# Optimization experiments

Measured on AMD Instinct MI355X. Metric: run time of the kernel, lower is better.

Reference implementation:

```python
import jax, jax.numpy as jnp
import numpy as np

B, C, N, DI, DC = 64, 32, 1152, 8, 16
ROUTINGS = 3


def squash(x, axis=-1):
    sq = jnp.sum(x * x, axis=axis, keepdims=True)
    scale = sq / (1.0 + sq) / jnp.sqrt(sq + 1e-07)
    return scale * x


def setup_inputs() -> dict:
    key = jax.random.key(0)
    k1, k2 = jax.random.split(key)
    inputs = jax.random.normal(k1, (B, N, DI), dtype=jnp.float32)
    # Xavier-uniform init for W[n_caps, n_in, d_cap, d_in]; fan computed over last two dims
    limit = float(np.sqrt(6.0 / (DC + DI)))
    W = jax.random.uniform(k2, (C, N, DC, DI), dtype=jnp.float32, minval=-limit, maxval=limit)
    return {"inputs": inputs, "W": W}


def reference(inputs, W):
    # inputs_hat[b,c,n,i] = sum_j W[c,n,i,j] * inputs[b,n,j]
    inputs_hat = jnp.einsum('cnij,bnj->bcni', W, inputs)  # [B,C,N,DC]
    b = jnp.zeros((B, C, N), dtype=inputs_hat.dtype)
    outputs = None
    for i in range(ROUTINGS):
        c = jax.nn.softmax(b, axis=1)                      # over output capsules
        s = jnp.einsum('bcn,bcni->bci', c, inputs_hat)     # weighted sum over input caps
        outputs = squash(s)                                # [B,C,DC]
        if i < ROUTINGS - 1:
            agreement = jnp.einsum('bci,bcni->bcn', outputs, inputs_hat)
            b = b + agreement
    return outputs
```

## Files before the change

### kernel.cpp

```cpp
#include <hip/hip_runtime.h>
#include <hip/hip_bf16.h>
#include <hip/hip_fp16.h>

#define B_  64
#define C_  32
#define N_  1152
#define DI_ 8
#define DC_ 16
#define STH 512

#define HCH 2
#define HSLOT 192
#define NOCT 24

#define FCH 3
#define FSLOT 128

static __device__ __forceinline__ unsigned pkh(float a, float b) {
    __half2 t = __float22half2_rn(make_float2(a, b));
    return *reinterpret_cast<unsigned*>(&t);
}
static __device__ __forceinline__ float2 uph(unsigned u) {
    __half2 h; *reinterpret_cast<unsigned*>(&h) = u;
    return __half22float2(h);
}

__global__ __launch_bounds__(STH, 4) void caps_hat(
    const float* __restrict__ X, const float* __restrict__ W,
    uint4* __restrict__ hatg, float* __restrict__ p1)
{
    __shared__ float wlds[HCH * 64 * 64];

    const int xcd  = blockIdx.x & 7;
    const int k    = blockIdx.x >> 3;
    const int bg   = k & 3;
    const int slot = 24 * xcd + (k >> 2);

    const int tid  = threadIdx.x;
    const int lane = tid & 63;
    const int c    = lane & 31;
    const int h    = lane >> 5;
    const int le   = 2 * c + h;
    const int sw   = c & 7;
    const int wu   = __builtin_amdgcn_readfirstlane(tid) >> 6;
    const int bl0  = wu * 2;

    float acc[2][8];
#pragma unroll
    for (int bq = 0; bq < 2; bq++)
#pragma unroll
        for (int r = 0; r < 8; r++) acc[bq][r] = 0.f;

    for (int cc = 0; cc < 3; cc++) {
        if (cc) __syncthreads();
        const int n0 = (slot + cc * HSLOT) * HCH;

#pragma unroll
        for (int G = tid; G < HCH * 1024; G += STH) {
            const int nl = G >> 10, f = (G >> 4) & 63, q = G & 15;
            const int wc = f >> 1, wh = f & 1;
            const float4 v = *(const float4*)(W + (size_t)(wc * N_ + n0 + nl) * 128 + wh * 64 + q * 4);
            *(float4*)(wlds + (nl * 64 + f) * 64 + (q ^ (wc & 7)) * 4) = v;
        }
        __syncthreads();

#pragma unroll
        for (int nl = 0; nl < HCH; nl++) {
            float4 xa[2], xb[2];
#pragma unroll
            for (int bq = 0; bq < 2; bq++) {
                const float* xp = X + ((size_t)(bg * 16 + bl0 + bq) * N_ + n0 + nl) * DI_;
                xa[bq] = *(const float4*)xp;
                xb[bq] = *(const float4*)(xp + 4);
            }
            uint4 hq[2];
            const float* frag = wlds + (nl * 64 + le) * 64;
#pragma unroll
            for (int rp = 0; rp < 4; rp++) {
                const int r0 = 2 * rp, r1 = r0 + 1;
                const int pa0 = ((2 * r0) ^ sw) * 4;
                const int pb0 = pa0 ^ 4;
                const int pa1 = ((2 * r1) ^ sw) * 4;
                const int pb1 = pa1 ^ 4;
                const float4 wa0 = *(const float4*)(frag + pa0);
                const float4 wb0 = *(const float4*)(frag + pb0);
                const float4 wa1 = *(const float4*)(frag + pa1);
                const float4 wb1 = *(const float4*)(frag + pb1);
#pragma unroll
                for (int bq = 0; bq < 2; bq++) {
                    const float hv0 = wa0.x*xa[bq].x + wa0.y*xa[bq].y + wa0.z*xa[bq].z + wa0.w*xa[bq].w
                                    + wb0.x*xb[bq].x + wb0.y*xb[bq].y + wb0.z*xb[bq].z + wb0.w*xb[bq].w;
                    const float hv1 = wa1.x*xa[bq].x + wa1.y*xa[bq].y + wa1.z*xa[bq].z + wa1.w*xa[bq].w
                                    + wb1.x*xb[bq].x + wb1.y*xb[bq].y + wb1.z*xb[bq].z + wb1.w*xb[bq].w;
                    acc[bq][r0] += hv0;
                    acc[bq][r1] += hv1;
                    (&hq[bq].x)[rp] = pkh(hv0, hv1);
                }
            }
#pragma unroll
            for (int bq = 0; bq < 2; bq++) {
                const int b = bg * 16 + bl0 + bq;
                hatg[(size_t)(b * N_ + n0 + nl) * 64 + le] = hq[bq];
            }
        }
    }

    float* pout = p1 + (size_t)(bg * HSLOT + slot) * (16 * 512);
#pragma unroll
    for (int bq = 0; bq < 2; bq++) {
        float* pb = pout + (bl0 + bq) * 512 + le * 8;
        *(float4*)pb       = make_float4(acc[bq][0]*0.03125f, acc[bq][1]*0.03125f,
                                         acc[bq][2]*0.03125f, acc[bq][3]*0.03125f);
        *(float4*)(pb + 4) = make_float4(acc[bq][4]*0.03125f, acc[bq][5]*0.03125f,
                                         acc[bq][6]*0.03125f, acc[bq][7]*0.03125f);
    }
}

__global__ __launch_bounds__(STH, 4) void caps_route(
    const uint4* __restrict__ hatg, const float* __restrict__ accb,
    float* __restrict__ p2)
{
    __shared__ float red[8 * 512];
    const int xcd  = blockIdx.x & 7;
    const int rest = blockIdx.x >> 3;
    const int ug   = rest % 3;
    const int b    = rest / 3;
    const int u    = 8 * ug + xcd;
    const int tid  = threadIdx.x;
    const int w    = tid >> 6;
    const int lane = tid & 63;
    const int c    = lane & 31;
    const int h    = lane >> 5;
    const int le   = 2 * c + h;

    const float* ap = accb + (size_t)b * 512 + le * 8;
    const float4 a0 = *(const float4*)ap;
    const float4 a1 = *(const float4*)(ap + 4);

    const uint4* hb = hatg + (size_t)(b * N_ + u * 48) * 64 + le;

    uint4 v[6];
#pragma unroll
    for (int m = 0; m < 6; m++)
        v[m] = hb[(size_t)(w + 8 * m) * 64];

    float lg[6], sm[6];
#pragma unroll
    for (int m = 0; m < 6; m++) {
        const float2 f0 = uph(v[m].x);
        const float2 f1 = uph(v[m].y);
        const float2 f2 = uph(v[m].z);
        const float2 f3 = uph(v[m].w);
        lg[m] = f0.x*a0.x + f0.y*a0.y + f1.x*a0.z + f1.y*a0.w
              + f2.x*a1.x + f2.y*a1.y + f3.x*a1.z + f3.y*a1.w;
    }
#pragma unroll
    for (int m = 0; m < 6; m++) lg[m] += __shfl_xor(lg[m], 32, 64);
#pragma unroll
    for (int m = 0; m < 6; m++) { lg[m] = __expf(lg[m]); sm[m] = lg[m]; }
#pragma unroll
    for (int d = 16; d >= 1; d >>= 1)
#pragma unroll
        for (int m = 0; m < 6; m++) sm[m] += __shfl_xor(sm[m], d, 64);

    float acc[8] = {0.f,0.f,0.f,0.f,0.f,0.f,0.f,0.f};
#pragma unroll
    for (int m = 0; m < 6; m++) {
        const float sc = lg[m] * __builtin_amdgcn_rcpf(sm[m]);
        const float2 f0 = uph(v[m].x);
        const float2 f1 = uph(v[m].y);
        const float2 f2 = uph(v[m].z);
        const float2 f3 = uph(v[m].w);
        acc[0] += sc * f0.x; acc[1] += sc * f0.y;
        acc[2] += sc * f1.x; acc[3] += sc * f1.y;
        acc[4] += sc * f2.x; acc[5] += sc * f2.y;
        acc[6] += sc * f3.x; acc[7] += sc * f3.y;
    }
    *(float4*)(red + w * 512 + le * 8)     = make_float4(acc[0], acc[1], acc[2], acc[3]);
    *(float4*)(red + w * 512 + le * 8 + 4) = make_float4(acc[4], acc[5], acc[6], acc[7]);
    __syncthreads();
    float vs = 0.f;
#pragma unroll
    for (int s = 0; s < 8; s++) vs += red[s * 512 + tid];
    p2[(size_t)(b * NOCT + u) * 512 + tid] = vs;
}

__global__ __launch_bounds__(512) void caps_r1(
    const float* __restrict__ p1, float* __restrict__ accb,
    float* __restrict__ out, int t)
{
    const int b   = blockIdx.x >> 2;
    const int q   = blockIdx.x & 3;
    const int tid = threadIdx.x;
    const int e   = q * 128 + (tid >> 2);
    const int p   = tid & 3;
    const int bg  = b >> 4, bl = b & 15;
    const float* base = p1 + (size_t)bg * HSLOT * 8192 + (size_t)bl * 512 + e;
    float v = 0.f;
#pragma unroll 8
    for (int ch = p; ch < HSLOT; ch += 4)
        v += base[(size_t)ch * 8192];
    v += __shfl_xor(v, 1, 64);
    v += __shfl_xor(v, 2, 64);
    float sq = v * v;
#pragma unroll
    for (int m = 4; m <= 32; m <<= 1) sq += __shfl_xor(sq, m, 64);
    const float scale = sq / (1.f + sq) * rsqrtf(sq + 1e-7f);
    const float ov = v * scale;
    if (p == 0) {
        const int oidx = b * 512 + e;
        if (t == 2) out[oidx] = ov;
        else        accb[oidx] = (t == 0) ? ov : (accb[oidx] + ov);
    }
}

__global__ __launch_bounds__(512) void caps_r2(
    const float* __restrict__ p2, float* __restrict__ accb,
    float* __restrict__ out, int t)
{
    const int b = blockIdx.x;
    const int e = threadIdx.x;
    const float* base = p2 + (size_t)b * (NOCT * 512) + e;
    float v = 0.f;
#pragma unroll
    for (int s = 0; s < NOCT; s++) v += base[s * 512];
    float sq = v * v;
#pragma unroll
    for (int m = 1; m <= 8; m <<= 1) sq += __shfl_xor(sq, m, 64);
    const float scale = sq / (1.f + sq) * rsqrtf(sq + 1e-7f);
    const float ov = v * scale;
    const int oidx = b * 512 + e;
    if (t == 2) out[oidx] = ov;
    else        accb[oidx] += ov;
}

__global__ __launch_bounds__(STH, 2) void caps_s_fb(
    const float* __restrict__ X, const float* __restrict__ W,
    const float* __restrict__ aout, float* __restrict__ partials, int t)
{
    __shared__ float wlds[FCH * 64 * 64];
    __shared__ float xlds[FCH * 16 * 8];
    const int bg = blockIdx.x & 3, slot = blockIdx.x >> 2;
    const int tid = threadIdx.x, w = tid >> 6, lane = tid & 63;
    const int c = lane & 31, h = lane >> 5, bl0 = w * 2, sw = c & 7;
    float areg[2][8] = {};
    if (t > 0) {
#pragma unroll
        for (int bq = 0; bq < 2; bq++) {
            const float* ap = aout + (size_t)(bg * 16 + bl0 + bq) * 512 + c * 16 + h * 8;
            const float4 a0 = *(const float4*)ap; const float4 a1 = *(const float4*)(ap + 4);
            areg[bq][0]=a0.x; areg[bq][1]=a0.y; areg[bq][2]=a0.z; areg[bq][3]=a0.w;
            areg[bq][4]=a1.x; areg[bq][5]=a1.y; areg[bq][6]=a1.z; areg[bq][7]=a1.w;
        }
    }
    float acc[2][8];
#pragma unroll
    for (int bq = 0; bq < 2; bq++)
#pragma unroll
        for (int r = 0; r < 8; r++) acc[bq][r] = 0.f;
    for (int cc = 0; cc < 3; cc++) {
        if (cc) __syncthreads();
        const int n0 = (slot + cc * FSLOT) * FCH;
        for (int G = tid; G < FCH * 1024; G += STH) {
            const int nl = G >> 10, f = (G >> 4) & 63, q = G & 15;
            const int wc = f >> 1, wh = f & 1;
            const float4 v = *(const float4*)(W + (size_t)(wc * N_ + n0 + nl) * 128 + wh * 64 + q * 4);
            *(float4*)(wlds + (nl * 64 + f) * 64 + (q ^ (wc & 7)) * 4) = v;
        }
        if (tid < FCH * 32) {
            const int nl = tid >> 5, bl = (tid >> 1) & 15, qx = tid & 1;
            const float4 v = *(const float4*)(X + (size_t)((bg * 16 + bl) * N_ + n0 + nl) * DI_ + qx * 4);
            *(float4*)(xlds + (nl * 16 + bl) * 8 + qx * 4) = v;
        }
        __syncthreads();
#pragma unroll
        for (int nl = 0; nl < FCH; nl++) {
            float4 xa[2], xb[2];
#pragma unroll
            for (int bq = 0; bq < 2; bq++) {
                const float* xp = xlds + (nl * 16 + bl0 + bq) * 8;
                xa[bq] = *(const float4*)xp; xb[bq] = *(const float4*)(xp + 4);
            }
            float hat[2][8];
            const float* frag = wlds + (nl * 64 + 2 * c + h) * 64;
#pragma unroll
            for (int r = 0; r < 8; r++) {
                const int pa = ((2 * r) ^ sw) * 4; const int pb = pa ^ 4;
                const float4 wa = *(const float4*)(frag + pa);
                const float4 wb = *(const float4*)(frag + pb);
#pragma unroll
                for (int bq = 0; bq < 2; bq++)
                    hat[bq][r] = wa.x*xa[bq].x + wa.y*xa[bq].y + wa.z*xa[bq].z + wa.w*xa[bq].w
                               + wb.x*xb[bq].x + wb.y*xb[bq].y + wb.z*xb[bq].z + wb.w*xb[bq].w;
            }
#pragma unroll
            for (int bq = 0; bq < 2; bq++) {
                float softc;
                if (t > 0) {
                    float lg = hat[bq][0]*areg[bq][0] + hat[bq][1]*areg[bq][1]
                             + hat[bq][2]*areg[bq][2] + hat[bq][3]*areg[bq][3]
                             + hat[bq][4]*areg[bq][4] + hat[bq][5]*areg[bq][5]
                             + hat[bq][6]*areg[bq][6] + hat[bq][7]*areg[bq][7];
                    lg += __shfl_xor(lg, 32, 64);
                    const float e = __expf(lg);
                    float s = e;
#pragma unroll
                    for (int m = 16; m >= 1; m >>= 1) s += __shfl_xor(s, m, 64);
                    softc = e / s;
                } else softc = 1.0f / 32.0f;
#pragma unroll
                for (int r = 0; r < 8; r++) acc[bq][r] += softc * hat[bq][r];
            }
        }
    }
    float* pout = partials + (size_t)(bg * FSLOT + slot) * (16 * 512);
#pragma unroll
    for (int bq = 0; bq < 2; bq++) {
        float* pb = pout + (bl0 + bq) * 512 + c * 16 + h * 8;
        *(float4*)pb       = make_float4(acc[bq][0], acc[bq][1], acc[bq][2], acc[bq][3]);
        *(float4*)(pb + 4) = make_float4(acc[bq][4], acc[bq][5], acc[bq][6], acc[bq][7]);
    }
}

__global__ __launch_bounds__(256) void caps_r1_fb(
    const float* __restrict__ partials, float* __restrict__ accb,
    float* __restrict__ out, int t)
{
    const int b   = blockIdx.x >> 2;
    const int q   = blockIdx.x & 3;
    const int tid = threadIdx.x;
    const int e   = q * 128 + (tid >> 1);
    const int p   = tid & 1;
    const int bg  = b >> 4, bl = b & 15;
    const float* base = partials + (size_t)bg * FSLOT * 8192 + (size_t)bl * 512 + e;
    float v = 0.f;
#pragma unroll 8
    for (int ch = p; ch < FSLOT; ch += 2)
        v += base[(size_t)ch * 8192];
    v += __shfl_xor(v, 1, 64);
    float sq = v * v;
#pragma unroll
    for (int m = 2; m <= 16; m <<= 1) sq += __shfl_xor(sq, m, 64);
    const float scale = sq / (1.f + sq) * rsqrtf(sq + 1e-7f);
    const float ov = v * scale;
    if (p == 0) {
        const int oidx = b * 512 + e;
        if (t == 2) out[oidx] = ov;
        else        accb[oidx] = (t == 0) ? ov : (accb[oidx] + ov);
    }
}

extern "C" void kernel_launch(void* const* d_in, const int* in_sizes, int n_in,
                              void* d_out, int out_size, void* d_ws, size_t ws_size,
                              hipStream_t stream) {
    const float* X = (const float*)d_in[0];
    const float* W = (const float*)d_in[1];
    float* out = (float*)d_out;

    const size_t hat_b = (size_t)B_ * N_ * 512 * 2;
    const size_t p1_b  = (size_t)4 * HSLOT * 8192 * 4;
    const size_t p2_b  = (size_t)B_ * NOCT * 512 * 4;
    const size_t acc_b = (size_t)B_ * 512 * 4;

    if (ws_size >= hat_b + p1_b + p2_b + acc_b) {
        char* ws = (char*)d_ws;
        uint4* hatg = (uint4*)ws;
        float* p1   = (float*)(ws + hat_b);
        float* p2   = (float*)(ws + hat_b + p1_b);
        float* accb = (float*)(ws + hat_b + p1_b + p2_b);
        caps_hat  <<<768, STH, 0, stream>>>(X, W, hatg, p1);
        caps_r1   <<<256, 512, 0, stream>>>(p1, accb, out, 0);
        caps_route<<<B_ * NOCT, STH, 0, stream>>>(hatg, accb, p2);
        caps_r2   <<<64, 512, 0, stream>>>(p2, accb, out, 1);
        caps_route<<<B_ * NOCT, STH, 0, stream>>>(hatg, accb, p2);
        caps_r2   <<<64, 512, 0, stream>>>(p2, accb, out, 2);
    } else {
        float* partials = (float*)d_ws;
        float* accb = partials + (size_t)512 * 8192;
        for (int t = 0; t < 3; t++) {
            caps_s_fb<<<512, STH, 0, stream>>>(X, W, accb, partials, t);
            caps_r1_fb<<<256, 256, 0, stream>>>(partials, accb, out, t);
        }
    }
}
```

Measured before the change: 128.9 us.

## Recompute prediction vectors each routing pass instead of storing fp16 hat tensor

Drops the materialized fp16 inputs_hat buffer and the separate route/reduce kernels. Each of the three routing iterations now reruns a fused kernel that recomputes hat from W and X, applies the softmax-weighted accumulation in registers, and writes partials for the existing r1 reduction. This trades the large hat write and two hat reads for re-reading W (about 4.7 MB) and redoing the matvec in every pass. It also removes the fp16 rounding of hat.

```diff
diff --git a/kernel.cpp b/kernel.cpp
--- a/kernel.cpp
+++ b/kernel.cpp
@@ -11,23 +11,13 @@
 
 #define HCH 2
 #define HSLOT 192
-#define NOCT 24
 
 #define FCH 3
 #define FSLOT 128
 
-static __device__ __forceinline__ unsigned pkh(float a, float b) {
-    __half2 t = __float22half2_rn(make_float2(a, b));
-    return *reinterpret_cast<unsigned*>(&t);
-}
-static __device__ __forceinline__ float2 uph(unsigned u) {
-    __half2 h; *reinterpret_cast<unsigned*>(&h) = u;
-    return __half22float2(h);
-}
-
-__global__ __launch_bounds__(STH, 4) void caps_hat(
+__global__ __launch_bounds__(STH, 4) void caps_pass(
     const float* __restrict__ X, const float* __restrict__ W,
-    uint4* __restrict__ hatg, float* __restrict__ p1)
+    const float* __restrict__ accb, float* __restrict__ p1, int t)
 {
     __shared__ float wlds[HCH * 64 * 64];
 
@@ -45,6 +35,18 @@
     const int wu   = __builtin_amdgcn_readfirstlane(tid) >> 6;
     const int bl0  = wu * 2;
 
+    float areg[2][8];
+    if (t > 0) {
+#pragma unroll
+        for (int bq = 0; bq < 2; bq++) {
+            const float* ap = accb + (size_t)(bg * 16 + bl0 + bq) * 512 + le * 8;
+            const float4 a0 = *(const float4*)ap;
+            const float4 a1 = *(const float4*)(ap + 4);
+            areg[bq][0]=a0.x; areg[bq][1]=a0.y; areg[bq][2]=a0.z; areg[bq][3]=a0.w;
+            areg[bq][4]=a1.x; areg[bq][5]=a1.y; areg[bq][6]=a1.z; areg[bq][7]=a1.w;
+        }
+    }
+
     float acc[2][8];
 #pragma unroll
     for (int bq = 0; bq < 2; bq++)
@@ -73,7 +75,7 @@
                 xa[bq] = *(const float4*)xp;
                 xb[bq] = *(const float4*)(xp + 4);
             }
-            uint4 hq[2];
+            float hat[2][8];
             const float* frag = wlds + (nl * 64 + le) * 64;
 #pragma unroll
             for (int rp = 0; rp < 4; rp++) {
@@ -88,19 +90,43 @@
                 const float4 wb1 = *(const float4*)(frag + pb1);
 #pragma unroll
                 for (int bq = 0; bq < 2; bq++) {
-                    const float hv0 = wa0.x*xa[bq].x + wa0.y*xa[bq].y + wa0.z*xa[bq].z + wa0.w*xa[bq].w
-                                    + wb0.x*xb[bq].x + wb0.y*xb[bq].y + wb0.z*xb[bq].z + wb0.w*xb[bq].w;
-                    const float hv1 = wa1.x*xa[bq].x + wa1.y*xa[bq].y + wa1.z*xa[bq].z + wa1.w*xa[bq].w
-                                    + wb1.x*xb[bq].x + wb1.y*xb[bq].y + wb1.z*xb[bq].z + wb1.w*xb[bq].w;
-                    acc[bq][r0] += hv0;
-                    acc[bq][r1] += hv1;
-                    (&hq[bq].x)[rp] = pkh(hv0, hv1);
+                    hat[bq][r0] = wa0.x*xa[bq].x + wa0.y*xa[bq].y + wa0.z*xa[bq].z + wa0.w*xa[bq].w
+                                + wb0.x*xb[bq].x + wb0.y*xb[bq].y + wb0.z*xb[bq].z + wb0.w*xb[bq].w;
+                    hat[bq][r1] = wa1.x*xa[bq].x + wa1.y*xa[bq].y + wa1.z*xa[bq].z + wa1.w*xa[bq].w
+                                + wb1.x*xb[bq].x + wb1.y*xb[bq].y + wb1.z*xb[bq].z + wb1.w*xb[bq].w;
                 }
             }
-#pragma unroll
-            for (int bq = 0; bq < 2; bq++) {
-                const int b = bg * 16 + bl0 + bq;
-                hatg[(size_t)(b * N_ + n0 + nl) * 64 + le] = hq[bq];
+            if (t == 0) {
+#pragma unroll
+                for (int bq = 0; bq < 2; bq++)
+#pragma unroll
+                    for (int r = 0; r < 8; r++) acc[bq][r] += 0.03125f * hat[bq][r];
+            } else {
+                float lg0 = hat[0][0]*areg[0][0] + hat[0][1]*areg[0][1]
+                          + hat[0][2]*areg[0][2] + hat[0][3]*areg[0][3]
+                          + hat[0][4]*areg[0][4] + hat[0][5]*areg[0][5]
+                          + hat[0][6]*areg[0][6] + hat[0][7]*areg[0][7];
+                float lg1 = hat[1][0]*areg[1][0] + hat[1][1]*areg[1][1]
+                          + hat[1][2]*areg[1][2] + hat[1][3]*areg[1][3]
+                          + hat[1][4]*areg[1][4] + hat[1][5]*areg[1][5]
+                          + hat[1][6]*areg[1][6] + hat[1][7]*areg[1][7];
+                lg0 += __shfl_xor(lg0, 32, 64);
+                lg1 += __shfl_xor(lg1, 32, 64);
+                const float e0 = __expf(lg0);
+                const float e1 = __expf(lg1);
+                float s0 = e0, s1 = e1;
+#pragma unroll
+                for (int m = 16; m >= 1; m >>= 1) {
+                    s0 += __shfl_xor(s0, m, 64);
+                    s1 += __shfl_xor(s1, m, 64);
+                }
+                const float sc0 = e0 * __builtin_amdgcn_rcpf(s0);
+                const float sc1 = e1 * __builtin_amdgcn_rcpf(s1);
+#pragma unroll
+                for (int r = 0; r < 8; r++) {
+                    acc[0][r] += sc0 * hat[0][r];
+                    acc[1][r] += sc1 * hat[1][r];
+                }
             }
         }
     }
@@ -109,80 +135,9 @@
 #pragma unroll
     for (int bq = 0; bq < 2; bq++) {
         float* pb = pout + (bl0 + bq) * 512 + le * 8;
-        *(float4*)pb       = make_float4(acc[bq][0]*0.03125f, acc[bq][1]*0.03125f,
-                                         acc[bq][2]*0.03125f, acc[bq][3]*0.03125f);
-        *(float4*)(pb + 4) = make_float4(acc[bq][4]*0.03125f, acc[bq][5]*0.03125f,
-                                         acc[bq][6]*0.03125f, acc[bq][7]*0.03125f);
-    }
-}
-
-__global__ __launch_bounds__(STH, 4) void caps_route(
-    const uint4* __restrict__ hatg, const float* __restrict__ accb,
-    float* __restrict__ p2)
-{
-    __shared__ float red[8 * 512];
-    const int xcd  = blockIdx.x & 7;
-    const int rest = blockIdx.x >> 3;
-    const int ug   = rest % 3;
-    const int b    = rest / 3;
-    const int u    = 8 * ug + xcd;
-    const int tid  = threadIdx.x;
-    const int w    = tid >> 6;
-    const int lane = tid & 63;
-    const int c    = lane & 31;
-    const int h    = lane >> 5;
-    const int le   = 2 * c + h;
-
-    const float* ap = accb + (size_t)b * 512 + le * 8;
-    const float4 a0 = *(const float4*)ap;
-    const float4 a1 = *(const float4*)(ap + 4);
-
-    const uint4* hb = hatg + (size_t)(b * N_ + u * 48) * 64 + le;
-
-    uint4 v[6];
-#pragma unroll
-    for (int m = 0; m < 6; m++)
-        v[m] = hb[(size_t)(w + 8 * m) * 64];
-
-    float lg[6], sm[6];
-#pragma unroll
-    for (int m = 0; m < 6; m++) {
-        const float2 f0 = uph(v[m].x);
-        const float2 f1 = uph(v[m].y);
-        const float2 f2 = uph(v[m].z);
-        const float2 f3 = uph(v[m].w);
-        lg[m] = f0.x*a0.x + f0.y*a0.y + f1.x*a0.z + f1.y*a0.w
-              + f2.x*a1.x + f2.y*a1.y + f3.x*a1.z + f3.y*a1.w;
-    }
-#pragma unroll
-    for (int m = 0; m < 6; m++) lg[m] += __shfl_xor(lg[m], 32, 64);
-#pragma unroll
-    for (int m = 0; m < 6; m++) { lg[m] = __expf(lg[m]); sm[m] = lg[m]; }
-#pragma unroll
-    for (int d = 16; d >= 1; d >>= 1)
-#pragma unroll
-        for (int m = 0; m < 6; m++) sm[m] += __shfl_xor(sm[m], d, 64);
-
-    float acc[8] = {0.f,0.f,0.f,0.f,0.f,0.f,0.f,0.f};
-#pragma unroll
-    for (int m = 0; m < 6; m++) {
-        const float sc = lg[m] * __builtin_amdgcn_rcpf(sm[m]);
-        const float2 f0 = uph(v[m].x);
-        const float2 f1 = uph(v[m].y);
-        const float2 f2 = uph(v[m].z);
-        const float2 f3 = uph(v[m].w);
-        acc[0] += sc * f0.x; acc[1] += sc * f0.y;
-        acc[2] += sc * f1.x; acc[3] += sc * f1.y;
-        acc[4] += sc * f2.x; acc[5] += sc * f2.y;
-        acc[6] += sc * f3.x; acc[7] += sc * f3.y;
-    }
-    *(float4*)(red + w * 512 + le * 8)     = make_float4(acc[0], acc[1], acc[2], acc[3]);
-    *(float4*)(red + w * 512 + le * 8 + 4) = make_float4(acc[4], acc[5], acc[6], acc[7]);
-    __syncthreads();
-    float vs = 0.f;
-#pragma unroll
-    for (int s = 0; s < 8; s++) vs += red[s * 512 + tid];
-    p2[(size_t)(b * NOCT + u) * 512 + tid] = vs;
+        *(float4*)pb       = make_float4(acc[bq][0], acc[bq][1], acc[bq][2], acc[bq][3]);
+        *(float4*)(pb + 4) = make_float4(acc[bq][4], acc[bq][5], acc[bq][6], acc[bq][7]);
+    }
 }
 
 __global__ __launch_bounds__(512) void caps_r1(
@@ -214,26 +169,6 @@
     }
 }
 
-__global__ __launch_bounds__(512) void caps_r2(
-    const float* __restrict__ p2, float* __restrict__ accb,
-    float* __restrict__ out, int t)
-{
-    const int b = blockIdx.x;
-    const int e = threadIdx.x;
-    const float* base = p2 + (size_t)b * (NOCT * 512) + e;
-    float v = 0.f;
-#pragma unroll
-    for (int s = 0; s < NOCT; s++) v += base[s * 512];
-    float sq = v * v;
-#pragma unroll
-    for (int m = 1; m <= 8; m <<= 1) sq += __shfl_xor(sq, m, 64);
-    const float scale = sq / (1.f + sq) * rsqrtf(sq + 1e-7f);
-    const float ov = v * scale;
-    const int oidx = b * 512 + e;
-    if (t == 2) out[oidx] = ov;
-    else        accb[oidx] += ov;
-}
-
 __global__ __launch_bounds__(STH, 2) void caps_s_fb(
     const float* __restrict__ X, const float* __restrict__ W,
     const float* __restrict__ aout, float* __restrict__ partials, int t)
@@ -357,23 +292,17 @@
     const float* W = (const float*)d_in[1];
     float* out = (float*)d_out;
 
-    const size_t hat_b = (size_t)B_ * N_ * 512 * 2;
     const size_t p1_b  = (size_t)4 * HSLOT * 8192 * 4;
-    const size_t p2_b  = (size_t)B_ * NOCT * 512 * 4;
     const size_t acc_b = (size_t)B_ * 512 * 4;
 
-    if (ws_size >= hat_b + p1_b + p2_b + acc_b) {
+    if (ws_size >= p1_b + acc_b) {
         char* ws = (char*)d_ws;
-        uint4* hatg = (uint4*)ws;
-        float* p1   = (float*)(ws + hat_b);
-        float* p2   = (float*)(ws + hat_b + p1_b);
-        float* accb = (float*)(ws + hat_b + p1_b + p2_b);
-        caps_hat  <<<768, STH, 0, stream>>>(X, W, hatg, p1);
-        caps_r1   <<<256, 512, 0, stream>>>(p1, accb, out, 0);
-        caps_route<<<B_ * NOCT, STH, 0, stream>>>(hatg, accb, p2);
-        caps_r2   <<<64, 512, 0, stream>>>(p2, accb, out, 1);
-        caps_route<<<B_ * NOCT, STH, 0, stream>>>(hatg, accb, p2);
-        caps_r2   <<<64, 512, 0, stream>>>(p2, accb, out, 2);
+        float* p1   = (float*)ws;
+        float* accb = (float*)(ws + p1_b);
+        for (int t = 0; t < 3; t++) {
+            caps_pass<<<768, STH, 0, stream>>>(X, W, accb, p1, t);
+            caps_r1  <<<256, 512, 0, stream>>>(p1, accb, out, t);
+        }
     } else {
         float* partials = (float*)d_ws;
         float* accb = partials + (size_t)512 * 8192;
```

New measurement: 209.8 us. +62.8%, slower.

## Prefetch next W chunk into registers, store iteration-1 partials as fp16

Applied to the files above, without the earlier changes.

caps_hat now loads the next W chunk into registers while it computes on the current chunk in LDS, then writes it to LDS after a barrier. The aim is to hide global-load latency behind the FMA work. The per-slot partial sums p1 are stored as packed half2 instead of float, and caps_r1 is reworked to read and reduce half2 pairs, which halves that traffic. Launch bounds drop from 4 to 2 waves-per-EU hint, giving more registers at some cost in occupancy, and fp16 partials lose precision.

```diff
diff --git a/kernel.cpp b/kernel.cpp
--- a/kernel.cpp
+++ b/kernel.cpp
@@ -25,9 +25,9 @@
     return __half22float2(h);
 }
 
-__global__ __launch_bounds__(STH, 4) void caps_hat(
+__global__ __launch_bounds__(STH, 2) void caps_hat(
     const float* __restrict__ X, const float* __restrict__ W,
-    uint4* __restrict__ hatg, float* __restrict__ p1)
+    uint4* __restrict__ hatg, __half2* __restrict__ p1)
 {
     __shared__ float wlds[HCH * 64 * 64];
 
@@ -45,24 +45,42 @@
     const int wu   = __builtin_amdgcn_readfirstlane(tid) >> 6;
     const int bl0  = wu * 2;
 
+    const int g_nl[4] = { (tid) >> 10, (tid + 512) >> 10, (tid + 1024) >> 10, (tid + 1536) >> 10 };
+    const int g_f [4] = { (tid >> 4) & 63, ((tid + 512) >> 4) & 63, ((tid + 1024) >> 4) & 63, ((tid + 1536) >> 4) & 63 };
+    const int g_q  = tid & 15;
+
     float acc[2][8];
 #pragma unroll
     for (int bq = 0; bq < 2; bq++)
 #pragma unroll
         for (int r = 0; r < 8; r++) acc[bq][r] = 0.f;
 
+    float4 wreg[4];
+    {
+        const int n0 = slot * HCH;
+#pragma unroll
+        for (int i = 0; i < 4; i++) {
+            const int wc = g_f[i] >> 1, wh = g_f[i] & 1;
+            wreg[i] = *(const float4*)(W + (size_t)(wc * N_ + n0 + g_nl[i]) * 128 + wh * 64 + g_q * 4);
+        }
+#pragma unroll
+        for (int i = 0; i < 4; i++) {
+            const int wc = g_f[i] >> 1;
+            *(float4*)(wlds + (g_nl[i] * 64 + g_f[i]) * 64 + (g_q ^ (wc & 7)) * 4) = wreg[i];
+        }
+    }
+    __syncthreads();
+
     for (int cc = 0; cc < 3; cc++) {
-        if (cc) __syncthreads();
+        if (cc < 2) {
+            const int n0 = (slot + (cc + 1) * HSLOT) * HCH;
+#pragma unroll
+            for (int i = 0; i < 4; i++) {
+                const int wc = g_f[i] >> 1, wh = g_f[i] & 1;
+                wreg[i] = *(const float4*)(W + (size_t)(wc * N_ + n0 + g_nl[i]) * 128 + wh * 64 + g_q * 4);
+            }
+        }
         const int n0 = (slot + cc * HSLOT) * HCH;
-
-#pragma unroll
-        for (int G = tid; G < HCH * 1024; G += STH) {
-            const int nl = G >> 10, f = (G >> 4) & 63, q = G & 15;
-            const int wc = f >> 1, wh = f & 1;
-            const float4 v = *(const float4*)(W + (size_t)(wc * N_ + n0 + nl) * 128 + wh * 64 + q * 4);
-            *(float4*)(wlds + (nl * 64 + f) * 64 + (q ^ (wc & 7)) * 4) = v;
-        }
-        __syncthreads();
 
 #pragma unroll
         for (int nl = 0; nl < HCH; nl++) {
@@ -103,20 +121,31 @@
                 hatg[(size_t)(b * N_ + n0 + nl) * 64 + le] = hq[bq];
             }
         }
-    }
-
-    float* pout = p1 + (size_t)(bg * HSLOT + slot) * (16 * 512);
+
+        __syncthreads();
+        if (cc < 2) {
+#pragma unroll
+            for (int i = 0; i < 4; i++) {
+                const int wc = g_f[i] >> 1;
+                *(float4*)(wlds + (g_nl[i] * 64 + g_f[i]) * 64 + (g_q ^ (wc & 7)) * 4) = wreg[i];
+            }
+            __syncthreads();
+        }
+    }
+
+    __half2* pout = p1 + (size_t)(bg * HSLOT + slot) * (16 * 256);
 #pragma unroll
     for (int bq = 0; bq < 2; bq++) {
-        float* pb = pout + (bl0 + bq) * 512 + le * 8;
-        *(float4*)pb       = make_float4(acc[bq][0]*0.03125f, acc[bq][1]*0.03125f,
-                                         acc[bq][2]*0.03125f, acc[bq][3]*0.03125f);
-        *(float4*)(pb + 4) = make_float4(acc[bq][4]*0.03125f, acc[bq][5]*0.03125f,
-                                         acc[bq][6]*0.03125f, acc[bq][7]*0.03125f);
-    }
-}
-
-__global__ __launch_bounds__(STH, 4) void caps_route(
+        uint4 st;
+        st.x = pkh(acc[bq][0]*0.03125f, acc[bq][1]*0.03125f);
+        st.y = pkh(acc[bq][2]*0.03125f, acc[bq][3]*0.03125f);
+        st.z = pkh(acc[bq][4]*0.03125f, acc[bq][5]*0.03125f);
+        st.w = pkh(acc[bq][6]*0.03125f, acc[bq][7]*0.03125f);
+        *(uint4*)(pout + (bl0 + bq) * 256 + le * 4) = st;
+    }
+}
+
+__global__ __launch_bounds__(STH, 2) void caps_route(
     const uint4* __restrict__ hatg, const float* __restrict__ accb,
     float* __restrict__ p2)
 {
@@ -186,31 +215,36 @@
 }
 
 __global__ __launch_bounds__(512) void caps_r1(
-    const float* __restrict__ p1, float* __restrict__ accb,
+    const __half2* __restrict__ p1, float* __restrict__ accb,
     float* __restrict__ out, int t)
 {
     const int b   = blockIdx.x >> 2;
     const int q   = blockIdx.x & 3;
     const int tid = threadIdx.x;
-    const int e   = q * 128 + (tid >> 2);
-    const int p   = tid & 3;
+    const int ep  = tid >> 3;
+    const int p   = tid & 7;
     const int bg  = b >> 4, bl = b & 15;
-    const float* base = p1 + (size_t)bg * HSLOT * 8192 + (size_t)bl * 512 + e;
-    float v = 0.f;
+    const __half2* base = p1 + (size_t)bg * HSLOT * 4096 + bl * 256 + (q * 64 + ep);
+    float vx = 0.f, vy = 0.f;
 #pragma unroll 8
-    for (int ch = p; ch < HSLOT; ch += 4)
-        v += base[(size_t)ch * 8192];
-    v += __shfl_xor(v, 1, 64);
-    v += __shfl_xor(v, 2, 64);
-    float sq = v * v;
-#pragma unroll
-    for (int m = 4; m <= 32; m <<= 1) sq += __shfl_xor(sq, m, 64);
+    for (int ch = p; ch < HSLOT; ch += 8) {
+        const float2 f = __half22float2(base[(size_t)ch * 4096]);
+        vx += f.x; vy += f.y;
+    }
+    vx += __shfl_xor(vx, 1, 64);  vy += __shfl_xor(vy, 1, 64);
+    vx += __shfl_xor(vx, 2, 64);  vy += __shfl_xor(vy, 2, 64);
+    vx += __shfl_xor(vx, 4, 64);  vy += __shfl_xor(vy, 4, 64);
+    float sq = vx * vx + vy * vy;
+    sq += __shfl_xor(sq, 8, 64);
+    sq += __shfl_xor(sq, 16, 64);
+    sq += __shfl_xor(sq, 32, 64);
     const float scale = sq / (1.f + sq) * rsqrtf(sq + 1e-7f);
-    const float ov = v * scale;
     if (p == 0) {
-        const int oidx = b * 512 + e;
-        if (t == 2) out[oidx] = ov;
-        else        accb[oidx] = (t == 0) ? ov : (accb[oidx] + ov);
+        const int oidx = b * 512 + q * 128 + ep * 2;
+        const float ox = vx * scale, oy = vy * scale;
+        if (t == 2) { out[oidx] = ox; out[oidx + 1] = oy; }
+        else if (t == 0) { accb[oidx] = ox; accb[oidx + 1] = oy; }
+        else { accb[oidx] += ox; accb[oidx + 1] += oy; }
     }
 }
 
@@ -358,16 +392,16 @@
     float* out = (float*)d_out;
 
     const size_t hat_b = (size_t)B_ * N_ * 512 * 2;
-    const size_t p1_b  = (size_t)4 * HSLOT * 8192 * 4;
+    const size_t p1_b  = (size_t)4 * HSLOT * 4096 * 4;
     const size_t p2_b  = (size_t)B_ * NOCT * 512 * 4;
     const size_t acc_b = (size_t)B_ * 512 * 4;
 
     if (ws_size >= hat_b + p1_b + p2_b + acc_b) {
         char* ws = (char*)d_ws;
-        uint4* hatg = (uint4*)ws;
-        float* p1   = (float*)(ws + hat_b);
-        float* p2   = (float*)(ws + hat_b + p1_b);
-        float* accb = (float*)(ws + hat_b + p1_b + p2_b);
+        uint4*   hatg = (uint4*)ws;
+        __half2* p1   = (__half2*)(ws + hat_b);
+        float*   p2   = (float*)(ws + hat_b + p1_b);
+        float*   accb = (float*)(ws + hat_b + p1_b + p2_b);
         caps_hat  <<<768, STH, 0, stream>>>(X, W, hatg, p1);
         caps_r1   <<<256, 512, 0, stream>>>(p1, accb, out, 0);
         caps_route<<<B_ * NOCT, STH, 0, stream>>>(hatg, accb, p2);
```

Measured after the change: 144.1 us. 1.12x slower.
